# Kernel tuning notes

Hardware: AMD Instinct MI355X
Metric: run time of the kernel (lower is better)

## Reference

```python
import jax, jax.numpy as jnp
import numpy as np

B, N, D, H = 8, 128, 512, 16
DK = D // H


def setup_inputs() -> dict:
    key = jax.random.key(0)
    ks = jax.random.split(key, 10)
    s = 1.0 / np.sqrt(D)
    return {
        "query_node": jax.random.normal(ks[0], (B, N, D), jnp.float32),
        "value_node": jax.random.normal(ks[1], (B, N, D), jnp.float32),
        "key_edge": jax.random.normal(ks[2], (B, N, N, D), jnp.float32) * 0.1,
        "adj_matrix": jax.random.uniform(ks[3], (B, N, N), jnp.float32),  # nonneg distance matrix
        "mask": jnp.ones((B, N), jnp.int32),
        "Wq": jax.random.normal(ks[4], (D, D), jnp.float32) * s,
        "bq": jnp.zeros((D,), jnp.float32),
        "Wk": jax.random.normal(ks[5], (D, D), jnp.float32) * s,
        "bk": jnp.zeros((D,), jnp.float32),
        "Wv": jax.random.normal(ks[6], (D, D), jnp.float32) * s,
        "bv": jnp.zeros((D,), jnp.float32),
        "Wo": jax.random.normal(ks[7], (D, D), jnp.float32) * s,
        "bo": jnp.zeros((D,), jnp.float32),
        "We": jax.random.normal(ks[8], (D, D), jnp.float32) * s,
        "be": jnp.zeros((D,), jnp.float32),
        "att_lambda": jnp.asarray(0.1, jnp.float32),
    }


def reference(query_node, value_node, key_edge, adj_matrix, mask,
              Wq, bq, Wk, bk, Wv, bv, Wo, bo, We, be, att_lambda):
    b, n, d = query_node.shape
    mask1 = mask[:, None, :]  # [b,1,n], broadcasts over rows like mask.repeat(1,n,1)
    # attenuated distance matrix -> kernel (softmax(-x)); masked entries -> +inf -> 0 weight
    adj = att_lambda * adj_matrix
    adj = jnp.where(mask1 == 0, jnp.inf, adj)
    adj = jax.nn.softmax(-adj, axis=-1)  # [b,n,n]
    # projections
    q = (query_node @ Wq + bq).reshape(b, n, H, DK).transpose(0, 2, 1, 3)      # [b,h,n,dk]
    k = (key_edge @ Wk + bk).reshape(b, n, n, H, DK).transpose(0, 3, 1, 2, 4)  # [b,h,n,n,dk]
    v = (value_node @ Wv + bv).reshape(b, n, H, DK).transpose(0, 2, 1, 3)      # [b,h,n,dk]
    scale = 1.0 / jnp.sqrt(jnp.asarray(DK, q.dtype))
    out_scores = jnp.einsum('bhmd,bhmnd->bhmn', q, k) * scale
    in_scores = jnp.einsum('bhnd,bhmnd->bhnm', q, k) * scale
    kmask = (mask1[:, :, None, :] == 0)  # [b,1,1,n]; mask value only depends on last axis
    neg = jnp.asarray(-jnp.inf, q.dtype)
    out_attn = jax.nn.softmax(jnp.where(kmask, neg, out_scores), axis=-1)
    in_attn = jax.nn.softmax(jnp.where(kmask, neg, in_scores), axis=-1)
    # message = out_attn + in_attn - diag_embed(diagonal(out_attn))
    diag = jnp.einsum('bhii->bhi', out_attn)
    idx = jnp.arange(n)
    message = (out_attn + in_attn).at[:, :, idx, idx].add(-diag)
    message = message * adj[:, None]  # adjacency gating, [b,h,n,n]
    node_hidden = jnp.einsum('bhmn,bhnd->bhmd', message, v)  # [b,h,n,dk]
    edge_hidden = message[..., None] * k                      # [b,h,m,n,dk]
    x = node_hidden.transpose(0, 2, 1, 3).reshape(b, n, d)
    e = edge_hidden.transpose(0, 2, 3, 1, 4).reshape(b, n, n, d)
    return (x @ Wo + bo, e @ We + be)
```

## Files before the change

kernel.cpp:

```cpp
#include <hip/hip_runtime.h>
#include <math.h>


using f32x4  = __attribute__((ext_vector_type(4))) float;
using bf16x8 = __attribute__((ext_vector_type(8))) short;

typedef const __attribute__((address_space(1))) unsigned int* gas_u32p;
typedef __attribute__((address_space(3))) unsigned int* las_u32p;

__device__ __forceinline__ void gll16(const void* gsrc, void* ldst) {
  __builtin_amdgcn_global_load_lds((gas_u32p)gsrc, (las_u32p)ldst, 16, 0, 0);
}

__device__ __forceinline__ unsigned short f2bf(float f) {
  union { float f; unsigned u; } v; v.f = f;
  unsigned u = v.u;
  u += 0x7FFFu + ((u >> 16) & 1u);
  return (unsigned short)(u >> 16);
}
__device__ __forceinline__ float bf2f(unsigned short h) {
  union { unsigned u; float f; } v; v.u = ((unsigned)h) << 16; return v.f;
}
__device__ __forceinline__ unsigned pack2(float lo, float hi) {
  union { float f; unsigned u; } a, b; a.f = lo; b.f = hi;
  return __builtin_amdgcn_perm(b.u + 0x8000u, a.u + 0x8000u, 0x07060302u);
}
__device__ __forceinline__ unsigned scale_pair(unsigned u, float mv) {
  union { unsigned u; float f; } lo, hi;
  lo.u = u << 16; hi.u = u & 0xFFFF0000u;
  float a = lo.f * mv, b = hi.f * mv;
  return pack2(a, b);
}

__global__ __launch_bounds__(256) void wt_kernel(const float* __restrict__ W,
                                                 unsigned short* __restrict__ WT) {
  __shared__ unsigned short T[64][72];
  int tile = blockIdx.x;
  int ti = tile >> 3, tj = tile & 7;
  int k0 = ti * 64, n0 = tj * 64;
  int t = threadIdx.x;
  int r = t >> 2, cq = (t & 3) * 16;
  const float* src = W + (size_t)(k0 + r) * 512 + n0 + cq;
#pragma unroll
  for (int j = 0; j < 16; ++j) T[r][cq + j] = f2bf(src[j]);
  __syncthreads();
  int c = t >> 2, rq = (t & 3) * 16;
  unsigned short* dst = WT + (size_t)(n0 + c) * 512 + k0 + rq;
#pragma unroll
  for (int j = 0; j < 16; ++j) dst[j] = T[rq + j][c];
}

__global__ __launch_bounds__(256) void adj_kernel(const float* __restrict__ adjm,
                                                  const int* __restrict__ mask,
                                                  const float* __restrict__ lam_p,
                                                  float* __restrict__ adjsm) {
  int row = blockIdx.x * 4 + (threadIdx.x >> 6);
  int lane = threadIdx.x & 63;
  int b = row >> 7;
  float lam = lam_p[0];
  const float* src = adjm + (size_t)row * 128;
  int m0 = mask[b * 128 + lane], m1 = mask[b * 128 + 64 + lane];
  float x0 = m0 ? -lam * src[lane] : -INFINITY;
  float x1 = m1 ? -lam * src[64 + lane] : -INFINITY;
  float mx = fmaxf(x0, x1);
#pragma unroll
  for (int o = 32; o; o >>= 1) mx = fmaxf(mx, __shfl_xor(mx, o));
  float e0 = __expf(x0 - mx), e1 = __expf(x1 - mx);
  float s = e0 + e1;
#pragma unroll
  for (int o = 32; o; o >>= 1) s += __shfl_xor(s, o);
  float inv = 1.0f / s;
  adjsm[(size_t)row * 128 + lane] = e0 * inv;
  adjsm[(size_t)row * 128 + 64 + lane] = e1 * inv;
}

__global__ __launch_bounds__(256) void gemm_kernel(const float* __restrict__ A,
                                                   const unsigned short* __restrict__ WT,
                                                   const float* __restrict__ bias,
                                                   float* __restrict__ C) {
  __shared__ unsigned short As[128 * 40];
  __shared__ unsigned short Bs[128 * 40];
  const int bid = blockIdx.x;
  const int rb = bid >> 2, cb = bid & 3;
  const int t = threadIdx.x;
  const int row0 = rb * 128, col0 = cb * 128;
  const int wave = t >> 6, lane = t & 63;
  const int wm = wave >> 1, wn = wave & 1;
  const int l15 = lane & 15, q4 = lane >> 4;
  const int arow = t >> 1, ahalf = t & 1;

  f32x4 acc[4][4];
#pragma unroll
  for (int i = 0; i < 4; ++i)
#pragma unroll
    for (int j = 0; j < 4; ++j)
#pragma unroll
      for (int r = 0; r < 4; ++r) acc[i][j][r] = 0.0f;

  for (int ki = 0; ki < 16; ++ki) {
    const int k0 = ki * 32;
    {
      const float* src = A + (size_t)(row0 + arow) * 512 + k0 + ahalf * 16;
      f32x4 v0 = *(const f32x4*)(src + 0);
      f32x4 v1 = *(const f32x4*)(src + 4);
      f32x4 v2 = *(const f32x4*)(src + 8);
      f32x4 v3 = *(const f32x4*)(src + 12);
      union { unsigned short u[16]; uint4 q[2]; } w;
#pragma unroll
      for (int j = 0; j < 4; ++j) {
        w.u[j] = f2bf(v0[j]); w.u[4 + j] = f2bf(v1[j]);
        w.u[8 + j] = f2bf(v2[j]); w.u[12 + j] = f2bf(v3[j]);
      }
      unsigned short* d = &As[arow * 40 + ahalf * 16];
      *(uint4*)d = w.q[0];
      *(uint4*)(d + 8) = w.q[1];
    }
    {
      const unsigned short* src = WT + (size_t)(col0 + arow) * 512 + k0 + ahalf * 16;
      uint4 p0 = *(const uint4*)src;
      uint4 p1 = *(const uint4*)(src + 8);
      unsigned short* d = &Bs[arow * 40 + ahalf * 16];
      *(uint4*)d = p0;
      *(uint4*)(d + 8) = p1;
    }
    __syncthreads();
    bf16x8 af[4], bfr[4];
#pragma unroll
    for (int mt = 0; mt < 4; ++mt)
      af[mt] = *(const bf16x8*)&As[(wm * 64 + mt * 16 + l15) * 40 + q4 * 8];
#pragma unroll
    for (int nt = 0; nt < 4; ++nt)
      bfr[nt] = *(const bf16x8*)&Bs[(wn * 64 + nt * 16 + l15) * 40 + q4 * 8];
#pragma unroll
    for (int mt = 0; mt < 4; ++mt)
#pragma unroll
      for (int nt = 0; nt < 4; ++nt)
        acc[mt][nt] = __builtin_amdgcn_mfma_f32_16x16x32_bf16(af[mt], bfr[nt], acc[mt][nt], 0, 0, 0);
    __syncthreads();
  }
#pragma unroll
  for (int mt = 0; mt < 4; ++mt) {
#pragma unroll
    for (int nt = 0; nt < 4; ++nt) {
      int gcol = col0 + wn * 64 + nt * 16 + l15;
      float bv = bias[gcol];
#pragma unroll
      for (int r = 0; r < 4; ++r) {
        int grow = row0 + wm * 64 + mt * 16 + q4 * 4 + r;
        C[(size_t)grow * 512 + gcol] = acc[mt][nt][r] + bv;
      }
    }
  }
}

template <int AMODE>
__global__ __launch_bounds__(256, 2) void gemm2_kernel(
    const void* __restrict__ Aptr, const unsigned short* __restrict__ WT,
    const float* __restrict__ bias, void* __restrict__ Cptr,
    const float* __restrict__ msg) {
  constexpr int DEPTH  = (AMODE == 2) ? 3 : 2;
  constexpr int ABYTES = (AMODE == 2) ? 8192 : 16384;
  constexpr int STAGEB = ABYTES + 16384;
  extern __shared__ char smem[];
  float* Msh = (float*)(smem + DEPTH * STAGEB);

  const int bid = blockIdx.x;
  const int rb = bid >> 1, cb = bid & 1;
  const int row0 = rb * 128, col0 = cb * 256;
  const int t = threadIdx.x;
  const int wave = t >> 6, lane = t & 63;
  const int wm = wave >> 1, wn = wave & 1;
  const int l15 = lane & 15, q4 = lane >> 4;

  f32x4 acc[4][8];
#pragma unroll
  for (int i = 0; i < 4; ++i)
#pragma unroll
    for (int j = 0; j < 8; ++j)
#pragma unroll
      for (int r = 0; r < 4; ++r) acc[i][j][r] = 0.0f;

  auto STAGE = [&](int ki, int s) {
    const int k0 = ki * 32;
    char* sa = smem + s * STAGEB;
    if (AMODE != 2) {
      const float* A = (const float*)Aptr;
      float* Asf = (float*)sa;
#pragma unroll
      for (int c = 0; c < 4; ++c) {
        int ar = (wave * 4 + c) * 8 + (lane >> 3);
        int p = (lane & 7) >> 1, h = lane & 1;
        int gcol = ((p ^ (ar & 3)) << 3) + (h << 2);
        gll16(A + (size_t)(row0 + ar) * 512 + k0 + gcol,
              Asf + (size_t)(wave * 4 + c) * 256);
      }
    } else {
      const unsigned short* A = (const unsigned short*)Aptr;
      unsigned short* Abf = (unsigned short*)sa;
#pragma unroll
      for (int c = 0; c < 2; ++c) {
        int ar = (wave * 2 + c) * 16 + (lane >> 2);
        int gq = (lane & 3) ^ (ar & 3);
        gll16(A + (size_t)(row0 + ar) * 512 + k0 + gq * 8,
              Abf + (size_t)(wave * 2 + c) * 512);
      }
    }
    unsigned short* Bsb = (unsigned short*)(sa + ABYTES);
#pragma unroll
    for (int c = 0; c < 4; ++c) {
      int br = (wave * 4 + c) * 16 + (lane >> 2);
      int gq = (lane & 3) ^ (br & 3);
      gll16(WT + (size_t)(col0 + br) * 512 + k0 + gq * 8,
            Bsb + (size_t)(wave * 4 + c) * 512);
    }
  };

  if (AMODE == 2) {
    int b = row0 >> 14, m = (row0 >> 7) & 127;
    size_t msbase = (size_t)(b * 16) * 16384 + (size_t)m * 128;
    int h = t >> 4, n8 = (t & 15) * 8;
    const float* mp = msg + msbase + (size_t)h * 16384 + n8;
    f32x4 m0 = *(const f32x4*)mp;
    f32x4 m1 = *(const f32x4*)(mp + 4);
    *(f32x4*)&Msh[h * 128 + n8] = m0;
    *(f32x4*)&Msh[h * 128 + n8 + 4] = m1;
    __syncthreads();
  }

  STAGE(0, 0);
  if (DEPTH == 3) STAGE(1, 1);

#pragma unroll
  for (int ki = 0; ki < 16; ++ki) {
    if (DEPTH == 3) {
      if (ki < 15) asm volatile("s_waitcnt vmcnt(6)" ::: "memory");
      else         asm volatile("s_waitcnt vmcnt(0)" ::: "memory");
    } else {
      asm volatile("s_waitcnt vmcnt(0)" ::: "memory");
    }
    __builtin_amdgcn_s_barrier();
    __builtin_amdgcn_sched_barrier(0);
    if (ki + DEPTH - 1 < 16) STAGE(ki + DEPTH - 1, (ki + DEPTH - 1) % DEPTH);

    char* sc = smem + (ki % DEPTH) * STAGEB;
    unsigned short* Bs = (unsigned short*)(sc + ABYTES);
    bf16x8 bfr[8], af[4];
#pragma unroll
    for (int nt = 0; nt < 8; ++nt) {
      int brow = wn * 128 + nt * 16 + l15;
      bfr[nt] = *(const bf16x8*)&Bs[brow * 32 + ((q4 ^ (brow & 3)) << 3)];
    }
    if (AMODE != 2) {
      float* Asf = (float*)sc;
#pragma unroll
      for (int mt = 0; mt < 4; ++mt) {
        int arow = wm * 64 + mt * 16 + l15;
        const float* ap = &Asf[arow * 32 + ((q4 ^ (arow & 3)) << 3)];
        f32x4 v0 = *(const f32x4*)ap;
        f32x4 v1 = *(const f32x4*)(ap + 4);
        union { unsigned d[4]; bf16x8 v; } u;
        u.d[0] = pack2(v0[0], v0[1]); u.d[1] = pack2(v0[2], v0[3]);
        u.d[2] = pack2(v1[0], v1[1]); u.d[3] = pack2(v1[2], v1[3]);
        af[mt] = u.v;
      }
    } else {
      unsigned short* Abf = (unsigned short*)sc;
#pragma unroll
      for (int mt = 0; mt < 4; ++mt) {
        int arow = wm * 64 + mt * 16 + l15;
        union { unsigned d[4]; bf16x8 v; } u;
        u.v = *(const bf16x8*)&Abf[arow * 32 + ((q4 ^ (arow & 3)) << 3)];
        float mv = Msh[ki * 128 + arow];
        u.d[0] = scale_pair(u.d[0], mv);
        u.d[1] = scale_pair(u.d[1], mv);
        u.d[2] = scale_pair(u.d[2], mv);
        u.d[3] = scale_pair(u.d[3], mv);
        af[mt] = u.v;
      }
    }
#pragma unroll
    for (int mt = 0; mt < 4; ++mt)
#pragma unroll
      for (int nt = 0; nt < 8; ++nt)
        acc[mt][nt] = __builtin_amdgcn_mfma_f32_16x16x32_bf16(af[mt], bfr[nt], acc[mt][nt], 0, 0, 0);
  }
#pragma unroll
  for (int mt = 0; mt < 4; ++mt) {
#pragma unroll
    for (int nt = 0; nt < 8; ++nt) {
      int gcol = col0 + wn * 128 + nt * 16 + l15;
      float bv = bias[gcol];
#pragma unroll
      for (int r = 0; r < 4; ++r) {
        int grow = row0 + wm * 64 + mt * 16 + q4 * 4 + r;
        float val = acc[mt][nt][r] + bv;
        if (AMODE == 1)
          ((unsigned short*)Cptr)[(size_t)grow * 512 + gcol] = f2bf(val);
        else
          ((float*)Cptr)[(size_t)grow * 512 + gcol] = val;
      }
    }
  }
}

__global__ __launch_bounds__(512) void scores_kernel(const unsigned short* __restrict__ Kbf,
                                                     const float* __restrict__ qw,
                                                     const int* __restrict__ mask,
                                                     float* __restrict__ sout,
                                                     float* __restrict__ sinT) {
  __shared__ float lso[16 * 9];
  __shared__ float lsi[16 * 9];
  const int bm = blockIdx.x;
  const int b = bm >> 7;
  const int t = threadIdx.x;
  const int wave = t >> 6, lane = t & 63;
  const float scale = 0.17677669529663687f;
  const int maskm = mask[bm];
  float qmr[8];
  {
    const float* qp = qw + (size_t)bm * 512 + lane * 8;
    f32x4 a = *(const f32x4*)qp, bq = *(const f32x4*)(qp + 4);
#pragma unroll
    for (int j = 0; j < 4; ++j) { qmr[j] = a[j]; qmr[4 + j] = bq[j]; }
  }
  for (int it = 0; it < 16; ++it) {
    int n = it * 8 + wave;
    const unsigned short* kp = Kbf + ((size_t)bm * 128 + n) * 512 + lane * 8;
    uint4 kv = *(const uint4*)kp;
    const float* qnp = qw + ((size_t)(b * 128 + n)) * 512 + lane * 8;
    f32x4 qa = *(const f32x4*)qnp, qb = *(const f32x4*)(qnp + 4);
    float qnr[8];
#pragma unroll
    for (int j = 0; j < 4; ++j) { qnr[j] = qa[j]; qnr[4 + j] = qb[j]; }
    unsigned vals[4] = {kv.x, kv.y, kv.z, kv.w};
    float so = 0.f, si = 0.f;
#pragma unroll
    for (int j = 0; j < 4; ++j) {
      float k0 = bf2f((unsigned short)(vals[j] & 0xFFFFu));
      float k1 = bf2f((unsigned short)(vals[j] >> 16));
      so += qmr[2 * j] * k0 + qmr[2 * j + 1] * k1;
      si += qnr[2 * j] * k0 + qnr[2 * j + 1] * k1;
    }
    so += __shfl_xor(so, 1); so += __shfl_xor(so, 2);
    si += __shfl_xor(si, 1); si += __shfl_xor(si, 2);
    int maskn = mask[b * 128 + n];
    if ((lane & 3) == 0) {
      int h = lane >> 2;
      lso[h * 9 + wave] = maskn ? so * scale : -INFINITY;
      lsi[h * 9 + wave] = maskm ? si * scale : -INFINITY;
    }
    __syncthreads();
    if (t < 256) {
      int sel = t >> 7, u = t & 127, h = u >> 3, w = u & 7;
      float v = sel ? lsi[h * 9 + w] : lso[h * 9 + w];
      float* dst = sel ? sinT : sout;
      dst[((size_t)(b * 16 + h) * 128 + (bm & 127)) * 128 + it * 8 + w] = v;
    }
    __syncthreads();
  }
}

__global__ __launch_bounds__(256) void tr128_kernel(const float* __restrict__ src,
                                                    float* __restrict__ dst) {
  __shared__ float T[64][65];
  int bid = blockIdx.x;
  int mat = bid >> 2, tile = bid & 3;
  int ti = tile >> 1, tj = tile & 1;
  const float* s = src + (size_t)mat * 16384;
  float* d = dst + (size_t)mat * 16384;
  int t = threadIdx.x;
  int r = t >> 2, cq = (t & 3) * 16;
#pragma unroll
  for (int j = 0; j < 16; ++j) T[r][cq + j] = s[(size_t)(ti * 64 + r) * 128 + tj * 64 + cq + j];
  __syncthreads();
  int c = t >> 2, rq = (t & 3) * 16;
#pragma unroll
  for (int j = 0; j < 16; ++j) d[(size_t)(tj * 64 + c) * 128 + ti * 64 + rq + j] = T[rq + j][c];
}

__global__ __launch_bounds__(256) void rsm_kernel(float* __restrict__ x) {
  int row = blockIdx.x * 4 + (threadIdx.x >> 6);
  int lane = threadIdx.x & 63;
  float* p = x + (size_t)row * 128;
  float a0 = p[lane], a1 = p[lane + 64];
  float mx = fmaxf(a0, a1);
#pragma unroll
  for (int o = 32; o; o >>= 1) mx = fmaxf(mx, __shfl_xor(mx, o));
  float e0 = __expf(a0 - mx), e1 = __expf(a1 - mx);
  float s = e0 + e1;
#pragma unroll
  for (int o = 32; o; o >>= 1) s += __shfl_xor(s, o);
  float inv = 1.0f / s;
  p[lane] = e0 * inv;
  p[lane + 64] = e1 * inv;
}

__global__ __launch_bounds__(256) void msg_kernel(const float* __restrict__ outat,
                                                  float* __restrict__ inat_msg,
                                                  const float* __restrict__ adjsm) {
  size_t idx = (size_t)blockIdx.x * 256 + threadIdx.x;
  int c = (int)(idx & 127), r = (int)((idx >> 7) & 127);
  int bh = (int)(idx >> 14), b = bh >> 4;
  float o = outat[idx], in = inat_msg[idx];
  float mv = (r == c) ? in : (o + in);
  mv *= adjsm[((size_t)b * 128 + r) * 128 + c];
  inat_msg[idx] = mv;
}

__global__ __launch_bounds__(256) void node_kernel(const float* __restrict__ msg,
                                                   const float* __restrict__ vw,
                                                   float* __restrict__ xpre) {
  __shared__ float V[128 * 36];
  __shared__ float Mg[64 * 132];
  int bid = blockIdx.x;
  int bh = bid >> 1, half = bid & 1;
  int b = bh >> 4, h = bh & 15;
  int t = threadIdx.x;
#pragma unroll
  for (int i = 0; i < 16; ++i) {
    int idx = t + i * 256;
    int j = idx >> 5, dk = idx & 31;
    V[j * 36 + dk] = vw[((size_t)b * 128 + j) * 512 + h * 32 + dk];
  }
  const float* mrow = msg + (size_t)bh * 16384 + (size_t)half * 64 * 128;
#pragma unroll
  for (int i = 0; i < 32; ++i) {
    int idx = t + i * 256;
    int r = idx >> 7, c = idx & 127;
    Mg[r * 132 + c] = mrow[idx];
  }
  __syncthreads();
  int il = t >> 2, d0 = (t & 3) * 8;
  float acc[8] = {0, 0, 0, 0, 0, 0, 0, 0};
  for (int j = 0; j < 128; ++j) {
    float mv = Mg[il * 132 + j];
#pragma unroll
    for (int d = 0; d < 8; ++d) acc[d] += mv * V[j * 36 + d0 + d];
  }
  float* xp = xpre + ((size_t)b * 128 + half * 64 + il) * 512 + h * 32 + d0;
#pragma unroll
  for (int d = 0; d < 8; ++d) xp[d] = acc[d];
}

extern "C" void kernel_launch(void* const* d_in, const int* in_sizes, int n_in,
                              void* d_out, int out_size, void* d_ws, size_t ws_size,
                              hipStream_t stream) {
  const float* q_node   = (const float*)d_in[0];
  const float* v_node   = (const float*)d_in[1];
  const float* key_edge = (const float*)d_in[2];
  const float* adjm     = (const float*)d_in[3];
  const int*   mask     = (const int*)d_in[4];
  const float* Wq = (const float*)d_in[5];
  const float* bq = (const float*)d_in[6];
  const float* Wk = (const float*)d_in[7];
  const float* bk = (const float*)d_in[8];
  const float* Wv = (const float*)d_in[9];
  const float* bv = (const float*)d_in[10];
  const float* Wo = (const float*)d_in[11];
  const float* bo = (const float*)d_in[12];
  const float* We = (const float*)d_in[13];
  const float* be = (const float*)d_in[14];
  const float* lam = (const float*)d_in[15];

  char* ws = (char*)d_ws;
  unsigned short* Kbf   = (unsigned short*)(ws);
  float* sout  = (float*)(ws + 134217728);
  float* sinT  = (float*)(ws + 142606336);
  float* msgb  = (float*)(ws + 150994944);
  float* adjsm = (float*)(ws + 159383552);
  float* qw    = (float*)(ws + 159907840);
  float* vw    = (float*)(ws + 162004992);
  float* xpre  = (float*)(ws + 164102144);
  unsigned short* WqT = (unsigned short*)(ws + 166199296);
  unsigned short* WkT = WqT + 262144;
  unsigned short* WvT = WkT + 262144;
  unsigned short* WoT = WvT + 262144;
  unsigned short* WeT = WoT + 262144;

  float* out_x = (float*)d_out;
  float* out_e = out_x + 524288;

  wt_kernel<<<64, 256, 0, stream>>>(Wq, WqT);
  wt_kernel<<<64, 256, 0, stream>>>(Wk, WkT);
  wt_kernel<<<64, 256, 0, stream>>>(Wv, WvT);
  wt_kernel<<<64, 256, 0, stream>>>(Wo, WoT);
  wt_kernel<<<64, 256, 0, stream>>>(We, WeT);
  adj_kernel<<<256, 256, 0, stream>>>(adjm, mask, lam, adjsm);

  gemm_kernel<<<32, 256, 0, stream>>>(q_node, WqT, bq, qw);
  gemm_kernel<<<32, 256, 0, stream>>>(v_node, WvT, bv, vw);
  gemm2_kernel<1><<<2048, 256, 65536, stream>>>(key_edge, WkT, bk, Kbf, nullptr);

  scores_kernel<<<1024, 512, 0, stream>>>(Kbf, qw, mask, sout, sinT);
  tr128_kernel<<<512, 256, 0, stream>>>(sinT, msgb);
  rsm_kernel<<<4096, 256, 0, stream>>>(sout);
  rsm_kernel<<<4096, 256, 0, stream>>>(msgb);
  msg_kernel<<<8192, 256, 0, stream>>>(sout, msgb, adjsm);
  node_kernel<<<256, 256, 0, stream>>>(msgb, vw, xpre);

  gemm_kernel<<<32, 256, 0, stream>>>(xpre, WoT, bo, out_x);
  gemm2_kernel<2><<<2048, 256, 81920, stream>>>(Kbf, WeT, be, out_e, msgb);
}
```

Before: 771.7 us.

## Fuse key projection with score computation and merge small launch kernels

```diff
diff --git a/kernel.cpp b/kernel.cpp
--- a/kernel.cpp
+++ b/kernel.cpp
@@ -32,10 +32,18 @@
   return pack2(a, b);
 }
 
-__global__ __launch_bounds__(256) void wt_kernel(const float* __restrict__ W,
-                                                 unsigned short* __restrict__ WT) {
+__global__ __launch_bounds__(256) void wt5_kernel(
+    const float* __restrict__ W0, const float* __restrict__ W1,
+    const float* __restrict__ W2, const float* __restrict__ W3,
+    const float* __restrict__ W4,
+    unsigned short* __restrict__ T0, unsigned short* __restrict__ T1,
+    unsigned short* __restrict__ T2, unsigned short* __restrict__ T3,
+    unsigned short* __restrict__ T4) {
   __shared__ unsigned short T[64][72];
-  int tile = blockIdx.x;
+  int mat = blockIdx.x >> 6;
+  const float* W = (mat == 0) ? W0 : (mat == 1) ? W1 : (mat == 2) ? W2 : (mat == 3) ? W3 : W4;
+  unsigned short* WT = (mat == 0) ? T0 : (mat == 1) ? T1 : (mat == 2) ? T2 : (mat == 3) ? T3 : T4;
+  int tile = blockIdx.x & 63;
   int ti = tile >> 3, tj = tile & 7;
   int k0 = ti * 64, n0 = tj * 64;
   int t = threadIdx.x;
@@ -74,14 +82,12 @@
   adjsm[(size_t)row * 128 + 64 + lane] = e1 * inv;
 }
 
-__global__ __launch_bounds__(256) void gemm_kernel(const float* __restrict__ A,
-                                                   const unsigned short* __restrict__ WT,
-                                                   const float* __restrict__ bias,
-                                                   float* __restrict__ C) {
+__device__ __forceinline__ void gemm_body(const float* __restrict__ A,
+                                          const unsigned short* __restrict__ WT,
+                                          const float* __restrict__ bias,
+                                          float* __restrict__ C, int rb, int cb) {
   __shared__ unsigned short As[128 * 40];
   __shared__ unsigned short Bs[128 * 40];
-  const int bid = blockIdx.x;
-  const int rb = bid >> 2, cb = bid & 3;
   const int t = threadIdx.x;
   const int row0 = rb * 128, col0 = cb * 128;
   const int wave = t >> 6, lane = t & 63;
@@ -153,13 +159,185 @@
   }
 }
 
-template <int AMODE>
-__global__ __launch_bounds__(256, 2) void gemm2_kernel(
-    const void* __restrict__ Aptr, const unsigned short* __restrict__ WT,
-    const float* __restrict__ bias, void* __restrict__ Cptr,
+__global__ __launch_bounds__(256) void gemm_kernel(const float* __restrict__ A,
+                                                   const unsigned short* __restrict__ WT,
+                                                   const float* __restrict__ bias,
+                                                   float* __restrict__ C) {
+  gemm_body(A, WT, bias, C, blockIdx.x >> 2, blockIdx.x & 3);
+}
+
+__global__ __launch_bounds__(256) void gemm_qv_kernel(
+    const float* __restrict__ A0, const unsigned short* __restrict__ W0,
+    const float* __restrict__ b0, float* __restrict__ C0,
+    const float* __restrict__ A1, const unsigned short* __restrict__ W1,
+    const float* __restrict__ b1, float* __restrict__ C1) {
+  int bid = blockIdx.x;
+  if (bid < 32) gemm_body(A0, W0, b0, C0, bid >> 2, bid & 3);
+  else { bid -= 32; gemm_body(A1, W1, b1, C1, bid >> 2, bid & 3); }
+}
+
+__global__ __launch_bounds__(512, 2) void kproj_scores_kernel(
+    const float* __restrict__ A, const unsigned short* __restrict__ WT,
+    const float* __restrict__ bias, unsigned short* __restrict__ Kbf,
+    const float* __restrict__ qw, const int* __restrict__ mask,
+    float* __restrict__ sout, float* __restrict__ sinT) {
+  constexpr int STAGEB = 16384 + 32768;
+  extern __shared__ char smem[];
+  const int bm = blockIdx.x;
+  const int row0 = bm << 7;
+  const int b = bm >> 7;
+  const int t = threadIdx.x;
+  const int wave = t >> 6, lane = t & 63;
+  const int wm = wave >> 2, wn = wave & 3;
+  const int l15 = lane & 15, q4 = lane >> 4;
+
+  f32x4 acc[4][8];
+#pragma unroll
+  for (int i = 0; i < 4; ++i)
+#pragma unroll
+    for (int j = 0; j < 8; ++j)
+#pragma unroll
+      for (int r = 0; r < 4; ++r) acc[i][j][r] = 0.0f;
+
+  auto STAGE = [&](int ki, int s) {
+    const int k0 = ki * 32;
+    char* sa = smem + s * STAGEB;
+    float* Asf = (float*)sa;
+#pragma unroll
+    for (int c = 0; c < 2; ++c) {
+      int ar = (wave * 2 + c) * 8 + (lane >> 3);
+      int p = (lane & 7) >> 1, h = lane & 1;
+      int gcol = ((p ^ (ar & 3)) << 3) + (h << 2);
+      gll16(A + (size_t)(row0 + ar) * 512 + k0 + gcol,
+            Asf + (size_t)(wave * 2 + c) * 256);
+    }
+    unsigned short* Bsb = (unsigned short*)(sa + 16384);
+#pragma unroll
+    for (int c = 0; c < 4; ++c) {
+      int br = (wave * 4 + c) * 16 + (lane >> 2);
+      int gq = (lane & 3) ^ (br & 3);
+      gll16(WT + (size_t)br * 512 + k0 + gq * 8,
+            Bsb + (size_t)(wave * 4 + c) * 512);
+    }
+  };
+
+  STAGE(0, 0);
+  STAGE(1, 1);
+
+#pragma unroll
+  for (int ki = 0; ki < 16; ++ki) {
+    if (ki < 15) asm volatile("s_waitcnt vmcnt(6)" ::: "memory");
+    else         asm volatile("s_waitcnt vmcnt(0)" ::: "memory");
+    __builtin_amdgcn_s_barrier();
+    __builtin_amdgcn_sched_barrier(0);
+    if (ki + 2 < 16) STAGE(ki + 2, (ki + 2) % 3);
+
+    char* sc = smem + (ki % 3) * STAGEB;
+    float* Asf = (float*)sc;
+    unsigned short* Bs = (unsigned short*)(sc + 16384);
+    bf16x8 bfr[8], af[4];
+#pragma unroll
+    for (int nt = 0; nt < 8; ++nt) {
+      int brow = wn * 128 + nt * 16 + l15;
+      bfr[nt] = *(const bf16x8*)&Bs[brow * 32 + ((q4 ^ (brow & 3)) << 3)];
+    }
+#pragma unroll
+    for (int mt = 0; mt < 4; ++mt) {
+      int arow = wm * 64 + mt * 16 + l15;
+      const float* ap = &Asf[arow * 32 + ((q4 ^ (arow & 3)) << 3)];
+      f32x4 v0 = *(const f32x4*)ap;
+      f32x4 v1 = *(const f32x4*)(ap + 4);
+      union { unsigned d[4]; bf16x8 v; } u;
+      u.d[0] = pack2(v0[0], v0[1]); u.d[1] = pack2(v0[2], v0[3]);
+      u.d[2] = pack2(v1[0], v1[1]); u.d[3] = pack2(v1[2], v1[3]);
+      af[mt] = u.v;
+    }
+#pragma unroll
+    for (int mt = 0; mt < 4; ++mt)
+#pragma unroll
+      for (int nt = 0; nt < 8; ++nt)
+        acc[mt][nt] = __builtin_amdgcn_mfma_f32_16x16x32_bf16(af[mt], bfr[nt], acc[mt][nt], 0, 0, 0);
+  }
+  __syncthreads();
+
+  unsigned short* K_lds = (unsigned short*)smem;
+  float* so_l = (float*)(smem + 131072);
+  float* si_l = so_l + 16 * 128;
+#pragma unroll
+  for (int mt = 0; mt < 4; ++mt) {
+#pragma unroll
+    for (int nt = 0; nt < 8; ++nt) {
+      int gcol = wn * 128 + nt * 16 + l15;
+      float bv = bias[gcol];
+#pragma unroll
+      for (int r = 0; r < 4; ++r) {
+        int gl = wm * 64 + mt * 16 + q4 * 4 + r;
+        unsigned short hv = f2bf(acc[mt][nt][r] + bv);
+        Kbf[(size_t)(row0 + gl) * 512 + gcol] = hv;
+        unsigned byteo = (unsigned)(gl * 1024) +
+                         ((2u * (unsigned)gcol) ^ (((unsigned)gl & 7u) << 4));
+        *(unsigned short*)((char*)K_lds + byteo) = hv;
+      }
+    }
+  }
+  __syncthreads();
+
+  const float scale = 0.17677669529663687f;
+  const int maskm = mask[bm];
+  float qmr[8];
+  {
+    const float* qp = qw + (size_t)bm * 512 + lane * 8;
+    f32x4 a = *(const f32x4*)qp, bq = *(const f32x4*)(qp + 4);
+#pragma unroll
+    for (int j = 0; j < 4; ++j) { qmr[j] = a[j]; qmr[4 + j] = bq[j]; }
+  }
+#pragma unroll
+  for (int it = 0; it < 16; ++it) {
+    int n = it * 8 + wave;
+    unsigned kbyte = (unsigned)(n * 1024) + (((unsigned)lane * 16u) ^ (((unsigned)n & 7u) << 4));
+    uint4 kv = *(const uint4*)((const char*)K_lds + kbyte);
+    const float* qnp = qw + (size_t)(b * 128 + n) * 512 + lane * 8;
+    f32x4 qa = *(const f32x4*)qnp, qb = *(const f32x4*)(qnp + 4);
+    float qnr[8];
+#pragma unroll
+    for (int j = 0; j < 4; ++j) { qnr[j] = qa[j]; qnr[4 + j] = qb[j]; }
+    unsigned vals[4] = {kv.x, kv.y, kv.z, kv.w};
+    float so = 0.f, si = 0.f;
+#pragma unroll
+    for (int j = 0; j < 4; ++j) {
+      float k0 = bf2f((unsigned short)(vals[j] & 0xFFFFu));
+      float k1 = bf2f((unsigned short)(vals[j] >> 16));
+      so += qmr[2 * j] * k0 + qmr[2 * j + 1] * k1;
+      si += qnr[2 * j] * k0 + qnr[2 * j + 1] * k1;
+    }
+    so += __shfl_xor(so, 1); so += __shfl_xor(so, 2);
+    si += __shfl_xor(si, 1); si += __shfl_xor(si, 2);
+    int maskn = mask[b * 128 + n];
+    if ((lane & 3) == 0) {
+      int h = lane >> 2;
+      int idx = h * 128 + (n ^ ((h & 7) << 2));
+      so_l[idx] = maskn ? so * scale : -INFINITY;
+      si_l[idx] = maskm ? si * scale : -INFINITY;
+    }
+  }
+  __syncthreads();
+  {
+    int h = t >> 5, c4 = (t & 31) * 4;
+    int idx = h * 128 + (c4 ^ ((h & 7) << 2));
+    f32x4 vo = *(const f32x4*)&so_l[idx];
+    f32x4 vi = *(const f32x4*)&si_l[idx];
+    size_t base = ((size_t)(b * 16 + h) * 128 + (size_t)(bm & 127)) * 128 + c4;
+    *(f32x4*)&sout[base] = vo;
+    *(f32x4*)&sinT[base] = vi;
+  }
+}
+
+__global__ __launch_bounds__(256, 2) void gemm2e_kernel(
+    const unsigned short* __restrict__ Aptr, const unsigned short* __restrict__ WT,
+    const float* __restrict__ bias, float* __restrict__ Cptr,
     const float* __restrict__ msg) {
-  constexpr int DEPTH  = (AMODE == 2) ? 3 : 2;
-  constexpr int ABYTES = (AMODE == 2) ? 8192 : 16384;
+  constexpr int DEPTH  = 3;
+  constexpr int ABYTES = 8192;
   constexpr int STAGEB = ABYTES + 16384;
   extern __shared__ char smem[];
   float* Msh = (float*)(smem + DEPTH * STAGEB);
@@ -183,27 +361,13 @@
   auto STAGE = [&](int ki, int s) {
     const int k0 = ki * 32;
     char* sa = smem + s * STAGEB;
-    if (AMODE != 2) {
-      const float* A = (const float*)Aptr;
-      float* Asf = (float*)sa;
-#pragma unroll
-      for (int c = 0; c < 4; ++c) {
-        int ar = (wave * 4 + c) * 8 + (lane >> 3);
-        int p = (lane & 7) >> 1, h = lane & 1;
-        int gcol = ((p ^ (ar & 3)) << 3) + (h << 2);
-        gll16(A + (size_t)(row0 + ar) * 512 + k0 + gcol,
-              Asf + (size_t)(wave * 4 + c) * 256);
-      }
-    } else {
-      const unsigned short* A = (const unsigned short*)Aptr;
-      unsigned short* Abf = (unsigned short*)sa;
-#pragma unroll
-      for (int c = 0; c < 2; ++c) {
-        int ar = (wave * 2 + c) * 16 + (lane >> 2);
-        int gq = (lane & 3) ^ (ar & 3);
-        gll16(A + (size_t)(row0 + ar) * 512 + k0 + gq * 8,
-              Abf + (size_t)(wave * 2 + c) * 512);
-      }
+    unsigned short* Abf = (unsigned short*)sa;
+#pragma unroll
+    for (int c = 0; c < 2; ++c) {
+      int ar = (wave * 2 + c) * 16 + (lane >> 2);
+      int gq = (lane & 3) ^ (ar & 3);
+      gll16(Aptr + (size_t)(row0 + ar) * 512 + k0 + gq * 8,
+            Abf + (size_t)(wave * 2 + c) * 512);
     }
     unsigned short* Bsb = (unsigned short*)(sa + ABYTES);
 #pragma unroll
@@ -215,7 +379,7 @@
     }
   };
 
-  if (AMODE == 2) {
+  {
     int b = row0 >> 14, m = (row0 >> 7) & 127;
     size_t msbase = (size_t)(b * 16) * 16384 + (size_t)m * 128;
     int h = t >> 4, n8 = (t & 15) * 8;
@@ -228,21 +392,17 @@
   }
 
   STAGE(0, 0);
-  if (DEPTH == 3) STAGE(1, 1);
+  STAGE(1, 1);
 
 #pragma unroll
   for (int ki = 0; ki < 16; ++ki) {
-    if (DEPTH == 3) {
-      if (ki < 15) asm volatile("s_waitcnt vmcnt(6)" ::: "memory");
-      else         asm volatile("s_waitcnt vmcnt(0)" ::: "memory");
-    } else {
-      asm volatile("s_waitcnt vmcnt(0)" ::: "memory");
-    }
+    if (ki < 15) asm volatile("s_waitcnt vmcnt(6)" ::: "memory");
+    else         asm volatile("s_waitcnt vmcnt(0)" ::: "memory");
     __builtin_amdgcn_s_barrier();
     __builtin_amdgcn_sched_barrier(0);
-    if (ki + DEPTH - 1 < 16) STAGE(ki + DEPTH - 1, (ki + DEPTH - 1) % DEPTH);
-
-    char* sc = smem + (ki % DEPTH) * STAGEB;
+    if (ki + 2 < 16) STAGE(ki + 2, (ki + 2) % 3);
+
+    char* sc = smem + (ki % 3) * STAGEB;
     unsigned short* Bs = (unsigned short*)(sc + ABYTES);
     bf16x8 bfr[8], af[4];
 #pragma unroll
@@ -250,33 +410,18 @@
       int brow = wn * 128 + nt * 16 + l15;
       bfr[nt] = *(const bf16x8*)&Bs[brow * 32 + ((q4 ^ (brow & 3)) << 3)];
     }
-    if (AMODE != 2) {
-      float* Asf = (float*)sc;
-#pragma unroll
-      for (int mt = 0; mt < 4; ++mt) {
-        int arow = wm * 64 + mt * 16 + l15;
-        const float* ap = &Asf[arow * 32 + ((q4 ^ (arow & 3)) << 3)];
-        f32x4 v0 = *(const f32x4*)ap;
-        f32x4 v1 = *(const f32x4*)(ap + 4);
-        union { unsigned d[4]; bf16x8 v; } u;
-        u.d[0] = pack2(v0[0], v0[1]); u.d[1] = pack2(v0[2], v0[3]);
-        u.d[2] = pack2(v1[0], v1[1]); u.d[3] = pack2(v1[2], v1[3]);
-        af[mt] = u.v;
-      }
-    } else {
-      unsigned short* Abf = (unsigned short*)sc;
-#pragma unroll
-      for (int mt = 0; mt < 4; ++mt) {
-        int arow = wm * 64 + mt * 16 + l15;
-        union { unsigned d[4]; bf16x8 v; } u;
-        u.v = *(const bf16x8*)&Abf[arow * 32 + ((q4 ^ (arow & 3)) << 3)];
-        float mv = Msh[ki * 128 + arow];
-        u.d[0] = scale_pair(u.d[0], mv);
-        u.d[1] = scale_pair(u.d[1], mv);
-        u.d[2] = scale_pair(u.d[2], mv);
-        u.d[3] = scale_pair(u.d[3], mv);
-        af[mt] = u.v;
-      }
+    unsigned short* Abf = (unsigned short*)sc;
+#pragma unroll
+    for (int mt = 0; mt < 4; ++mt) {
+      int arow = wm * 64 + mt * 16 + l15;
+      union { unsigned d[4]; bf16x8 v; } u;
+      u.v = *(const bf16x8*)&Abf[arow * 32 + ((q4 ^ (arow & 3)) << 3)];
+      float mv = Msh[ki * 128 + arow];
+      u.d[0] = scale_pair(u.d[0], mv);
+      u.d[1] = scale_pair(u.d[1], mv);
+      u.d[2] = scale_pair(u.d[2], mv);
+      u.d[3] = scale_pair(u.d[3], mv);
+      af[mt] = u.v;
     }
 #pragma unroll
     for (int mt = 0; mt < 4; ++mt)
@@ -293,70 +438,9 @@
 #pragma unroll
       for (int r = 0; r < 4; ++r) {
         int grow = row0 + wm * 64 + mt * 16 + q4 * 4 + r;
-        float val = acc[mt][nt][r] + bv;
-        if (AMODE == 1)
-          ((unsigned short*)Cptr)[(size_t)grow * 512 + gcol] = f2bf(val);
-        else
-          ((float*)Cptr)[(size_t)grow * 512 + gcol] = val;
+        Cptr[(size_t)grow * 512 + gcol] = acc[mt][nt][r] + bv;
       }
     }
-  }
-}
-
-__global__ __launch_bounds__(512) void scores_kernel(const unsigned short* __restrict__ Kbf,
-                                                     const float* __restrict__ qw,
-                                                     const int* __restrict__ mask,
-                                                     float* __restrict__ sout,
-                                                     float* __restrict__ sinT) {
-  __shared__ float lso[16 * 9];
-  __shared__ float lsi[16 * 9];
-  const int bm = blockIdx.x;
-  const int b = bm >> 7;
-  const int t = threadIdx.x;
-  const int wave = t >> 6, lane = t & 63;
-  const float scale = 0.17677669529663687f;
-  const int maskm = mask[bm];
-  float qmr[8];
-  {
-    const float* qp = qw + (size_t)bm * 512 + lane * 8;
-    f32x4 a = *(const f32x4*)qp, bq = *(const f32x4*)(qp + 4);
-#pragma unroll
-    for (int j = 0; j < 4; ++j) { qmr[j] = a[j]; qmr[4 + j] = bq[j]; }
-  }
-  for (int it = 0; it < 16; ++it) {
-    int n = it * 8 + wave;
-    const unsigned short* kp = Kbf + ((size_t)bm * 128 + n) * 512 + lane * 8;
-    uint4 kv = *(const uint4*)kp;
-    const float* qnp = qw + ((size_t)(b * 128 + n)) * 512 + lane * 8;
-    f32x4 qa = *(const f32x4*)qnp, qb = *(const f32x4*)(qnp + 4);
-    float qnr[8];
-#pragma unroll
-    for (int j = 0; j < 4; ++j) { qnr[j] = qa[j]; qnr[4 + j] = qb[j]; }
-    unsigned vals[4] = {kv.x, kv.y, kv.z, kv.w};
-    float so = 0.f, si = 0.f;
-#pragma unroll
-    for (int j = 0; j < 4; ++j) {
-      float k0 = bf2f((unsigned short)(vals[j] & 0xFFFFu));
-      float k1 = bf2f((unsigned short)(vals[j] >> 16));
-      so += qmr[2 * j] * k0 + qmr[2 * j + 1] * k1;
-      si += qnr[2 * j] * k0 + qnr[2 * j + 1] * k1;
-    }
-    so += __shfl_xor(so, 1); so += __shfl_xor(so, 2);
-    si += __shfl_xor(si, 1); si += __shfl_xor(si, 2);
-    int maskn = mask[b * 128 + n];
-    if ((lane & 3) == 0) {
-      int h = lane >> 2;
-      lso[h * 9 + wave] = maskn ? so * scale : -INFINITY;
-      lsi[h * 9 + wave] = maskm ? si * scale : -INFINITY;
-    }
-    __syncthreads();
-    if (t < 256) {
-      int sel = t >> 7, u = t & 127, h = u >> 3, w = u & 7;
-      float v = sel ? lsi[h * 9 + w] : lso[h * 9 + w];
-      float* dst = sel ? sinT : sout;
-      dst[((size_t)(b * 16 + h) * 128 + (bm & 127)) * 128 + it * 8 + w] = v;
-    }
-    __syncthreads();
   }
 }
 
@@ -378,33 +462,38 @@
   for (int j = 0; j < 16; ++j) d[(size_t)(tj * 64 + c) * 128 + ti * 64 + rq + j] = T[rq + j][c];
 }
 
-__global__ __launch_bounds__(256) void rsm_kernel(float* __restrict__ x) {
+__global__ __launch_bounds__(256) void smmsg_kernel(const float* __restrict__ sout,
+                                                    float* __restrict__ msgb,
+                                                    const float* __restrict__ adjsm) {
   int row = blockIdx.x * 4 + (threadIdx.x >> 6);
   int lane = threadIdx.x & 63;
-  float* p = x + (size_t)row * 128;
-  float a0 = p[lane], a1 = p[lane + 64];
-  float mx = fmaxf(a0, a1);
-#pragma unroll
-  for (int o = 32; o; o >>= 1) mx = fmaxf(mx, __shfl_xor(mx, o));
-  float e0 = __expf(a0 - mx), e1 = __expf(a1 - mx);
-  float s = e0 + e1;
-#pragma unroll
-  for (int o = 32; o; o >>= 1) s += __shfl_xor(s, o);
-  float inv = 1.0f / s;
-  p[lane] = e0 * inv;
-  p[lane + 64] = e1 * inv;
-}
-
-__global__ __launch_bounds__(256) void msg_kernel(const float* __restrict__ outat,
-                                                  float* __restrict__ inat_msg,
-                                                  const float* __restrict__ adjsm) {
-  size_t idx = (size_t)blockIdx.x * 256 + threadIdx.x;
-  int c = (int)(idx & 127), r = (int)((idx >> 7) & 127);
-  int bh = (int)(idx >> 14), b = bh >> 4;
-  float o = outat[idx], in = inat_msg[idx];
-  float mv = (r == c) ? in : (o + in);
-  mv *= adjsm[((size_t)b * 128 + r) * 128 + c];
-  inat_msg[idx] = mv;
+  int bh = row >> 7, b = bh >> 4, i = row & 127;
+  const float* op = sout + (size_t)row * 128;
+  float* ip = msgb + (size_t)row * 128;
+  float o0 = op[lane], o1 = op[lane + 64];
+  float i0 = ip[lane], i1 = ip[lane + 64];
+  float mo = fmaxf(o0, o1), mi = fmaxf(i0, i1);
+#pragma unroll
+  for (int o = 32; o; o >>= 1) {
+    mo = fmaxf(mo, __shfl_xor(mo, o));
+    mi = fmaxf(mi, __shfl_xor(mi, o));
+  }
+  float eo0 = __expf(o0 - mo), eo1 = __expf(o1 - mo);
+  float ei0 = __expf(i0 - mi), ei1 = __expf(i1 - mi);
+  float so = eo0 + eo1, si = ei0 + ei1;
+#pragma unroll
+  for (int o = 32; o; o >>= 1) {
+    so += __shfl_xor(so, o);
+    si += __shfl_xor(si, o);
+  }
+  float invo = 1.0f / so, invi = 1.0f / si;
+  float ao0 = eo0 * invo, ao1 = eo1 * invo;
+  float ai0 = ei0 * invi, ai1 = ei1 * invi;
+  float m0 = (lane == i) ? ai0 : (ao0 + ai0);
+  float m1 = (lane + 64 == i) ? ai1 : (ao1 + ai1);
+  const float* ar = adjsm + ((size_t)b * 128 + i) * 128;
+  ip[lane] = m0 * ar[lane];
+  ip[lane + 64] = m1 * ar[lane + 64];
 }
 
 __global__ __launch_bounds__(256) void node_kernel(const float* __restrict__ msg,
@@ -480,24 +569,18 @@
   float* out_x = (float*)d_out;
   float* out_e = out_x + 524288;
 
-  wt_kernel<<<64, 256, 0, stream>>>(Wq, WqT);
-  wt_kernel<<<64, 256, 0, stream>>>(Wk, WkT);
-  wt_kernel<<<64, 256, 0, stream>>>(Wv, WvT);
-  wt_kernel<<<64, 256, 0, stream>>>(Wo, WoT);
-  wt_kernel<<<64, 256, 0, stream>>>(We, WeT);
+  wt5_kernel<<<320, 256, 0, stream>>>(Wq, Wk, Wv, Wo, We, WqT, WkT, WvT, WoT, WeT);
   adj_kernel<<<256, 256, 0, stream>>>(adjm, mask, lam, adjsm);
 
-  gemm_kernel<<<32, 256, 0, stream>>>(q_node, WqT, bq, qw);
-  gemm_kernel<<<32, 256, 0, stream>>>(v_node, WvT, bv, vw);
-  gemm2_kernel<1><<<2048, 256, 65536, stream>>>(key_edge, WkT, bk, Kbf, nullptr);
-
-  scores_kernel<<<1024, 512, 0, stream>>>(Kbf, qw, mask, sout, sinT);
+  gemm_qv_kernel<<<64, 256, 0, stream>>>(q_node, WqT, bq, qw, v_node, WvT, bv, vw);
+
+  kproj_scores_kernel<<<1024, 512, 147456, stream>>>(key_edge, WkT, bk, Kbf,
+                                                     qw, mask, sout, sinT);
+
   tr128_kernel<<<512, 256, 0, stream>>>(sinT, msgb);
-  rsm_kernel<<<4096, 256, 0, stream>>>(sout);
-  rsm_kernel<<<4096, 256, 0, stream>>>(msgb);
-  msg_kernel<<<8192, 256, 0, stream>>>(sout, msgb, adjsm);
+  smmsg_kernel<<<4096, 256, 0, stream>>>(sout, msgb, adjsm);
   node_kernel<<<256, 256, 0, stream>>>(msgb, vw, xpre);
 
   gemm_kernel<<<32, 256, 0, stream>>>(xpre, WoT, bo, out_x);
-  gemm2_kernel<2><<<2048, 256, 81920, stream>>>(Kbf, WeT, be, out_e, msgb);
-}
+  gemm2e_kernel<<<2048, 256, 81920, stream>>>(Kbf, WeT, be, out_e, msgb);
+}
```

Measured after the change: 700.6 us. 9.2% less time.
